# Optimization experiments

Hardware: AMD Instinct MI355X
Metric: run time of the kernel (lower is better)

## Reference

```python
import jax, jax.numpy as jnp
import numpy as np

K = 11          # kernel_size / block size
C_CONST = 0.0009
B, CH, H, W = 16, 1, 1408, 1408


def _block_mean(x):
    # Non-overlapping KxK block average == conv2d(ones/K^2, stride=K, groups=C)
    b, c, h, w = x.shape
    return x.reshape(b, c, h // K, K, w // K, K).mean(axis=(3, 5))


def setup_inputs() -> dict:
    key = jax.random.key(0)
    k1, k2, k3 = jax.random.split(key, 3)
    shape = (B, CH, H, W)
    return {
        "vis_images": jax.random.uniform(k1, shape, dtype=jnp.float32),
        "ir_images": jax.random.uniform(k2, shape, dtype=jnp.float32),
        "fusion_images": jax.random.uniform(k3, shape, dtype=jnp.float32),
    }


def reference(vis_images, ir_images, fusion_images):
    vm = _block_mean(vis_images)
    vv = jnp.abs(_block_mean(vis_images ** 2) - vm ** 2)
    im = _block_mean(ir_images)
    iv = jnp.abs(_block_mean(ir_images ** 2) - im ** 2)
    fm = _block_mean(fusion_images)
    fv = jnp.abs(_block_mean(fusion_images ** 2) - fm ** 2)
    vf_cov = _block_mean(vis_images * fusion_images) - vm * fm
    if_cov = _block_mean(ir_images * fusion_images) - im * fm
    c = C_CONST
    ssim_l_vf = (2 * vm * fm + c) / (vm ** 2 + fm ** 2 + c)
    ssim_l_if = (2 * im * fm + c) / (im ** 2 + fm ** 2 + c)
    ssim_s_vf = (vf_cov + c) / (vv + fv + c)
    ssim_s_if = (if_cov + c) / (iv + fv + c)
    score = jnp.where(vm > im, ssim_l_vf * ssim_s_vf, ssim_l_if * ssim_s_if)
    return 1.0 - score.mean()
```

## Files before the change

### kernel.cpp

```cpp
#include <hip/hip_runtime.h>


namespace {
constexpr int K      = 11;
constexpr int W      = 1408;
constexpr int H      = 1408;
constexpr int B      = 16;
constexpr int BPR    = W / K;
constexpr int BROWS  = H / K;
constexpr int CHUNKS = W / 4;
constexpr float C_C  = 0.0009f;
constexpr float INV_KK = 1.0f / (float)(K * K);
}

__device__ __forceinline__ void acc4(float4& a, const float4 v) {
    a.x += v.x; a.y += v.y; a.z += v.z; a.w += v.w;
}
__device__ __forceinline__ void fma4(float4& a, const float4 u, const float4 v) {
    a.x += u.x * v.x; a.y += u.y * v.y; a.z += u.z * v.z; a.w += u.w * v.w;
}

__global__ __launch_bounds__(256) void vif_pass1(
    const float* __restrict__ vis,
    const float* __restrict__ ir,
    const float* __restrict__ fus,
    double* __restrict__ accum)
{
    __shared__ float s[8][W];
    __shared__ float wsum[4];

    const int t  = threadIdx.x;
    const int b  = blockIdx.x >> 7;
    const int br = blockIdx.x & 127;
    const size_t base = (size_t)b * ((size_t)H * W) + (size_t)br * K * W;

    for (int c = t; c < CHUNKS; c += 256) {
        float4 sv  = make_float4(0.f, 0.f, 0.f, 0.f);
        float4 sv2 = make_float4(0.f, 0.f, 0.f, 0.f);
        float4 si  = make_float4(0.f, 0.f, 0.f, 0.f);
        float4 si2 = make_float4(0.f, 0.f, 0.f, 0.f);
        float4 sf  = make_float4(0.f, 0.f, 0.f, 0.f);
        float4 sf2 = make_float4(0.f, 0.f, 0.f, 0.f);
        float4 svf = make_float4(0.f, 0.f, 0.f, 0.f);
        float4 sif = make_float4(0.f, 0.f, 0.f, 0.f);
        const size_t off = base + (size_t)c * 4;
#pragma unroll
        for (int r = 0; r < K; ++r) {
            const size_t o = off + (size_t)r * W;
            const float4 v = *(const float4*)(vis + o);
            const float4 i = *(const float4*)(ir  + o);
            const float4 f = *(const float4*)(fus + o);
            acc4(sv, v);
            fma4(sv2, v, v);
            acc4(si, i);
            fma4(si2, i, i);
            acc4(sf, f);
            fma4(sf2, f, f);
            fma4(svf, v, f);
            fma4(sif, i, f);
        }
        const int col = c * 4;
        *(float4*)&s[0][col] = sv;
        *(float4*)&s[1][col] = sv2;
        *(float4*)&s[2][col] = si;
        *(float4*)&s[3][col] = si2;
        *(float4*)&s[4][col] = sf;
        *(float4*)&s[5][col] = sf2;
        *(float4*)&s[6][col] = svf;
        *(float4*)&s[7][col] = sif;
    }
    __syncthreads();

    float score = 0.0f;
    if (t < BPR) {
        float a0 = 0.f, a1 = 0.f, a2 = 0.f, a3 = 0.f;
        float a4 = 0.f, a5 = 0.f, a6 = 0.f, a7 = 0.f;
        const int c0 = t * K;
#pragma unroll
        for (int k = 0; k < K; ++k) {
            a0 += s[0][c0 + k];
            a1 += s[1][c0 + k];
            a2 += s[2][c0 + k];
            a3 += s[3][c0 + k];
            a4 += s[4][c0 + k];
            a5 += s[5][c0 + k];
            a6 += s[6][c0 + k];
            a7 += s[7][c0 + k];
        }
        const float vm  = a0 * INV_KK;
        const float vs2 = a1 * INV_KK;
        const float im  = a2 * INV_KK;
        const float is2 = a3 * INV_KK;
        const float fm  = a4 * INV_KK;
        const float fs2 = a5 * INV_KK;
        const float vfm = a6 * INV_KK;
        const float ifm = a7 * INV_KK;

        const float vv = fabsf(vs2 - vm * vm);
        const float iv = fabsf(is2 - im * im);
        const float fv = fabsf(fs2 - fm * fm);
        const float vf_cov = vfm - vm * fm;
        const float if_cov = ifm - im * fm;

        const float l_vf = (2.f * vm * fm + C_C) / (vm * vm + fm * fm + C_C);
        const float l_if = (2.f * im * fm + C_C) / (im * im + fm * fm + C_C);
        const float s_vf = (vf_cov + C_C) / (vv + fv + C_C);
        const float s_if = (if_cov + C_C) / (iv + fv + C_C);

        score = (vm > im) ? (l_vf * s_vf) : (l_if * s_if);
    }

#pragma unroll
    for (int o = 32; o > 0; o >>= 1) score += __shfl_down(score, o, 64);
    if ((t & 63) == 0) wsum[t >> 6] = score;
    __syncthreads();
    if (t == 0) {
        const double tot = (double)(wsum[0] + wsum[1] + wsum[2] + wsum[3]);
        atomicAdd(accum, tot);
    }
}

__global__ void vif_finalize(const double* __restrict__ accum,
                             float* __restrict__ out)
{
    if (threadIdx.x == 0 && blockIdx.x == 0) {
        out[0] = 1.0f - (float)(accum[0] / (double)(B * BROWS * BPR));
    }
}

extern "C" void kernel_launch(void* const* d_in, const int* in_sizes, int n_in,
                              void* d_out, int out_size, void* d_ws, size_t ws_size,
                              hipStream_t stream) {
    const float* vis = (const float*)d_in[0];
    const float* ir  = (const float*)d_in[1];
    const float* fus = (const float*)d_in[2];
    float* out = (float*)d_out;
    double* accum = (double*)d_ws;

    hipMemsetAsync(accum, 0, sizeof(double), stream);
    vif_pass1<<<dim3(B * BROWS), dim3(256), 0, stream>>>(vis, ir, fus, accum);
    vif_finalize<<<dim3(1), dim3(64), 0, stream>>>(accum, out);
}
```

Measured before the change: 342.3 us.

## Use 384 threads, one float4 column each, with per-block split partial sums

```diff
diff --git a/kernel.cpp b/kernel.cpp
--- a/kernel.cpp
+++ b/kernel.cpp
@@ -20,21 +20,34 @@
     a.x += u.x * v.x; a.y += u.y * v.y; a.z += u.z * v.z; a.w += u.w * v.w;
 }
 
-__global__ __launch_bounds__(256) void vif_pass1(
+__device__ __forceinline__ void split4(const float4 a, const int nb,
+                                       float& l, float& r) {
+    l = a.x;
+    r = 0.f;
+    if (nb > 1) l += a.y; else r += a.y;
+    if (nb > 2) l += a.z; else r += a.z;
+    if (nb > 3) l += a.w; else r += a.w;
+}
+
+__global__ __launch_bounds__(384, 6) void vif_pass1(
     const float* __restrict__ vis,
     const float* __restrict__ ir,
     const float* __restrict__ fus,
     double* __restrict__ accum)
 {
-    __shared__ float s[8][W];
-    __shared__ float wsum[4];
+    __shared__ float s[8][4][BPR];
+    __shared__ float wsum[6];
 
     const int t  = threadIdx.x;
     const int b  = blockIdx.x >> 7;
     const int br = blockIdx.x & 127;
-    const size_t base = (size_t)b * ((size_t)H * W) + (size_t)br * K * W;
 
-    for (int c = t; c < CHUNKS; c += 256) {
+    for (int i = t; i < 8 * 4 * BPR; i += 384) ((float*)s)[i] = 0.f;
+    __syncthreads();
+
+    if (t < CHUNKS) {
+        const size_t base = (size_t)b * ((size_t)H * W) + (size_t)br * K * W
+                          + (size_t)t * 4;
         float4 sv  = make_float4(0.f, 0.f, 0.f, 0.f);
         float4 sv2 = make_float4(0.f, 0.f, 0.f, 0.f);
         float4 si  = make_float4(0.f, 0.f, 0.f, 0.f);
@@ -43,10 +56,9 @@
         float4 sf2 = make_float4(0.f, 0.f, 0.f, 0.f);
         float4 svf = make_float4(0.f, 0.f, 0.f, 0.f);
         float4 sif = make_float4(0.f, 0.f, 0.f, 0.f);
-        const size_t off = base + (size_t)c * 4;
 #pragma unroll
         for (int r = 0; r < K; ++r) {
-            const size_t o = off + (size_t)r * W;
+            const size_t o = base + (size_t)r * W;
             const float4 v = *(const float4*)(vis + o);
             const float4 i = *(const float4*)(ir  + o);
             const float4 f = *(const float4*)(fus + o);
@@ -59,42 +71,36 @@
             fma4(svf, v, f);
             fma4(sif, i, f);
         }
-        const int col = c * 4;
-        *(float4*)&s[0][col] = sv;
-        *(float4*)&s[1][col] = sv2;
-        *(float4*)&s[2][col] = si;
-        *(float4*)&s[3][col] = si2;
-        *(float4*)&s[4][col] = sf;
-        *(float4*)&s[5][col] = sf2;
-        *(float4*)&s[6][col] = svf;
-        *(float4*)&s[7][col] = sif;
+        const int bl = (4 * t) / K;
+        const int nb = K * (bl + 1) - 4 * t;
+        const int sl = t & 3;
+        float l, r;
+        split4(sv,  nb, l, r); s[0][sl][bl] = l; if (nb < 4) s[0][sl][bl + 1] = r;
+        split4(sv2, nb, l, r); s[1][sl][bl] = l; if (nb < 4) s[1][sl][bl + 1] = r;
+        split4(si,  nb, l, r); s[2][sl][bl] = l; if (nb < 4) s[2][sl][bl + 1] = r;
+        split4(si2, nb, l, r); s[3][sl][bl] = l; if (nb < 4) s[3][sl][bl + 1] = r;
+        split4(sf,  nb, l, r); s[4][sl][bl] = l; if (nb < 4) s[4][sl][bl + 1] = r;
+        split4(sf2, nb, l, r); s[5][sl][bl] = l; if (nb < 4) s[5][sl][bl + 1] = r;
+        split4(svf, nb, l, r); s[6][sl][bl] = l; if (nb < 4) s[6][sl][bl + 1] = r;
+        split4(sif, nb, l, r); s[7][sl][bl] = l; if (nb < 4) s[7][sl][bl + 1] = r;
     }
     __syncthreads();
 
     float score = 0.0f;
     if (t < BPR) {
-        float a0 = 0.f, a1 = 0.f, a2 = 0.f, a3 = 0.f;
-        float a4 = 0.f, a5 = 0.f, a6 = 0.f, a7 = 0.f;
-        const int c0 = t * K;
+        float a[8];
 #pragma unroll
-        for (int k = 0; k < K; ++k) {
-            a0 += s[0][c0 + k];
-            a1 += s[1][c0 + k];
-            a2 += s[2][c0 + k];
-            a3 += s[3][c0 + k];
-            a4 += s[4][c0 + k];
-            a5 += s[5][c0 + k];
-            a6 += s[6][c0 + k];
-            a7 += s[7][c0 + k];
-        }
-        const float vm  = a0 * INV_KK;
-        const float vs2 = a1 * INV_KK;
-        const float im  = a2 * INV_KK;
-        const float is2 = a3 * INV_KK;
-        const float fm  = a4 * INV_KK;
-        const float fs2 = a5 * INV_KK;
-        const float vfm = a6 * INV_KK;
-        const float ifm = a7 * INV_KK;
+        for (int q = 0; q < 8; ++q)
+            a[q] = s[q][0][t] + s[q][1][t] + s[q][2][t] + s[q][3][t];
+
+        const float vm  = a[0] * INV_KK;
+        const float vs2 = a[1] * INV_KK;
+        const float im  = a[2] * INV_KK;
+        const float is2 = a[3] * INV_KK;
+        const float fm  = a[4] * INV_KK;
+        const float fs2 = a[5] * INV_KK;
+        const float vfm = a[6] * INV_KK;
+        const float ifm = a[7] * INV_KK;
 
         const float vv = fabsf(vs2 - vm * vm);
         const float iv = fabsf(is2 - im * im);
@@ -115,7 +121,9 @@
     if ((t & 63) == 0) wsum[t >> 6] = score;
     __syncthreads();
     if (t == 0) {
-        const double tot = (double)(wsum[0] + wsum[1] + wsum[2] + wsum[3]);
+        double tot = 0.0;
+#pragma unroll
+        for (int wv = 0; wv < 6; ++wv) tot += (double)wsum[wv];
         atomicAdd(accum, tot);
     }
 }
@@ -138,6 +146,6 @@
     double* accum = (double*)d_ws;
 
     hipMemsetAsync(accum, 0, sizeof(double), stream);
-    vif_pass1<<<dim3(B * BROWS), dim3(256), 0, stream>>>(vis, ir, fus, accum);
+    vif_pass1<<<dim3(B * BROWS), dim3(384), 0, stream>>>(vis, ir, fus, accum);
     vif_finalize<<<dim3(1), dim3(64), 0, stream>>>(accum, out);
 }
```

After: 417.6 us. +22.0%, slower.
